# Kernel optimization log

Measured on AMD Instinct MI355X. Metric: run time of the kernel, lower is better.

## Reference

```python
import jax, jax.numpy as jnp
import numpy as np

IMAGE_W = 1024; IMAGE_H = 1024
STRIDES = (8, 16, 32, 64, 128)
TOP_N = 1000; MIN_SCORE = 0.01; NMS_THR = 0.6; MAX_DET = 100
BATCH = 16; NUM_CLASSES = 80


def setup_inputs():
    keys = jax.random.split(jax.random.key(0), 3 * len(STRIDES))
    inp = {}
    for l, s in enumerate(STRIDES):
        H, W = IMAGE_H // s, IMAGE_W // s
        inp[f"cls_head_{l}"] = jax.random.normal(keys[3 * l], (BATCH, H, W, NUM_CLASSES), jnp.float32)
        inp[f"reg_head_{l}"] = jax.random.normal(keys[3 * l + 1], (BATCH, H, W, 4), jnp.float32)
        inp[f"center_head_{l}"] = jax.random.normal(keys[3 * l + 2], (BATCH, H, W, 1), jnp.float32)
        xs = (jnp.arange(W, dtype=jnp.float32) + 0.5) * s
        ys = (jnp.arange(H, dtype=jnp.float32) + 0.5) * s
        gx, gy = jnp.meshgrid(xs, ys)  # each [H, W]
        pos = jnp.stack([gx, gy], axis=-1)  # [H, W, 2] = (ctr_x, ctr_y)
        inp[f"position_{l}"] = jnp.broadcast_to(pos, (BATCH, H, W, 2))
    return inp


def _decode_levels(cls_heads, reg_heads, center_heads, positions):
    S, C, R, P = [], [], [], []
    for cls, reg, ctr, pos in zip(cls_heads, reg_heads, center_heads, positions):
        B = cls.shape[0]
        cls = jax.nn.sigmoid(cls).reshape(B, -1, cls.shape[-1])  # [B,N,C]
        reg = jnp.exp(reg).reshape(B, -1, 4)
        ctr = jax.nn.sigmoid(ctr).reshape(B, -1)
        pos = pos.reshape(B, -1, 2)
        scores = jnp.sqrt(jnp.max(cls, axis=2) * ctr)  # sqrt(cls_max * centerness)
        classes = jnp.argmax(cls, axis=2)
        if scores.shape[1] >= TOP_N:
            scores, idx = jax.lax.top_k(scores, TOP_N)
            classes = jnp.take_along_axis(classes, idx, axis=1)
            reg = jnp.take_along_axis(reg, idx[:, :, None], axis=1)
            pos = jnp.take_along_axis(pos, idx[:, :, None], axis=1)
        S.append(scores); C.append(classes); R.append(reg); P.append(pos)
    return (jnp.concatenate(S, 1), jnp.concatenate(C, 1),
            jnp.concatenate(R, 1), jnp.concatenate(P, 1))


def _nms_keep(boxes, valid, iou_thr):
    # greedy class-agnostic NMS on score-descending boxes [N,4]
    N = boxes.shape[0]
    x1, y1, x2, y2 = boxes[:, 0], boxes[:, 1], boxes[:, 2], boxes[:, 3]
    areas = (x2 - x1) * (y2 - y1)
    idx = jnp.arange(N)

    def body(i, suppressed):
        keep_i = valid[i] & ~suppressed[i]
        xx1 = jnp.maximum(x1[i], x1); yy1 = jnp.maximum(y1[i], y1)
        xx2 = jnp.minimum(x2[i], x2); yy2 = jnp.minimum(y2[i], y2)
        inter = jnp.maximum(xx2 - xx1, 0.0) * jnp.maximum(yy2 - yy1, 0.0)
        iou = inter / (areas[i] + areas - inter)
        return suppressed | (keep_i & (iou > iou_thr) & (idx > i))

    suppressed = jax.lax.fori_loop(0, N, body, jnp.zeros((N,), bool))
    return valid & ~suppressed


def _per_image(scores, classes, reg, pos):
    xy_min = pos - reg[:, 0:2]
    xy_max = pos + reg[:, 2:4]
    boxes = jnp.concatenate([xy_min, xy_max], axis=1).astype(jnp.int32)  # trunc like .int()
    boxes = jnp.stack([jnp.maximum(boxes[:, 0], 0),
                       jnp.maximum(boxes[:, 1], 0),
                       jnp.minimum(boxes[:, 2], IMAGE_W - 1),
                       jnp.minimum(boxes[:, 3], IMAGE_H - 1)], axis=1).astype(jnp.float32)
    valid = scores > MIN_SCORE
    order = jnp.argsort(jnp.where(valid, -scores, jnp.inf))  # valid, score-descending first
    sb, ss = boxes[order], scores[order]
    sc, sv = classes[order].astype(jnp.float32), valid[order]
    kept = _nms_keep(sb, sv, NMS_THR)
    rank = jnp.cumsum(kept) - 1
    slot = jnp.where(kept, jnp.minimum(rank, MAX_DET), MAX_DET)  # overflow -> scratch slot
    out_s = jnp.full((MAX_DET + 1,), -1.0, jnp.float32).at[slot].set(jnp.where(kept, ss, -1.0))[:MAX_DET]
    out_c = jnp.full((MAX_DET + 1,), -1.0, jnp.float32).at[slot].set(jnp.where(kept, sc, -1.0))[:MAX_DET]
    out_b = jnp.full((MAX_DET + 1, 4), -1.0, jnp.float32).at[slot].set(jnp.where(kept[:, None], sb, -1.0))[:MAX_DET]
    return out_s, out_c, out_b


def _forward(cls_heads, reg_heads, center_heads, positions):
    s, c, r, p = _decode_levels(cls_heads, reg_heads, center_heads, positions)
    return jax.vmap(_per_image)(s, c, r, p)


def reference(cls_head_0, reg_head_0, center_head_0, position_0,
              cls_head_1, reg_head_1, center_head_1, position_1,
              cls_head_2, reg_head_2, center_head_2, position_2,
              cls_head_3, reg_head_3, center_head_3, position_3,
              cls_head_4, reg_head_4, center_head_4, position_4):
    cls_heads = [cls_head_0, cls_head_1, cls_head_2, cls_head_3, cls_head_4]
    reg_heads = [reg_head_0, reg_head_1, reg_head_2, reg_head_3, reg_head_4]
    center_heads = [center_head_0, center_head_1, center_head_2, center_head_3, center_head_4]
    positions = [position_0, position_1, position_2, position_3, position_4]
    return _forward(cls_heads, reg_heads, center_heads, positions)
```

## Files before the change

### kernel.cpp

```cpp
#include <hip/hip_runtime.h>
#include <stdint.h>

#define BATCH 16
#define NCLS 80
#define NPOS 21824
#define POOLN 3320
#define MAXDET 100

#define CAP0 4096
#define CAP1 2432
#define CAP2 1024
#define C34 320
#define SEG1 (CAP0)
#define SEG2 (CAP0 + CAP1)
#define SEG3 (CAP0 + CAP1 + CAP2)
#define CAPTOT (SEG3 + C34)

#define DEC_BPI 341
#define POS_BPI 13
#define NBINS 4096

__device__ const int d_lvl_off[5] = {0, 16384, 20480, 21504, 21760};
__device__ const int d_lvl_hw[5]  = {16384, 4096, 1024, 256, 64};

struct Ptrs { const float* p[20]; };

__device__ __forceinline__ void map_lvl(int r, int& level, int& hw) {
  if      (r < 16384) { level = 0; hw = r; }
  else if (r < 20480) { level = 1; hw = r - 16384; }
  else if (r < 21504) { level = 2; hw = r - 20480; }
  else if (r < 21760) { level = 3; hw = r - 21504; }
  else                { level = 4; hw = r - 21760; }
}


__global__ __launch_bounds__(256) void decode_kernel(Ptrs args, uint4* __restrict__ dec,
                                                     unsigned long long* __restrict__ gbuf,
                                                     unsigned* __restrict__ sbuf) {
  __shared__ float2 sm[1280];
  int b  = blockIdx.x / DEC_BPI;
  int bb = blockIdx.x - b * DEC_BPI;
  int t = threadIdx.x;

  int flat0 = bb * 64;
  int level, hw0;
  map_lvl(flat0, level, hw0);
  int HW = d_lvl_hw[level];

  const float* cls = args.p[level * 4 + 0];
  const float* reg = args.p[level * 4 + 1];
  const float* ctr = args.p[level * 4 + 2];
  const float* pos = args.p[level * 4 + 3];

  const float4* c4 = (const float4*)(cls + ((long)b * HW + hw0) * NCLS);
#pragma unroll
  for (int w = 0; w < 5; ++w) {
    int f = t + 256 * w;
    float4 v = c4[f];
    int q = f % 20;
    float m = -1e30f; int am = 4 * q;
    if (v.x > m) { m = v.x; am = 4 * q + 0; }
    if (v.y > m) { m = v.y; am = 4 * q + 1; }
    if (v.z > m) { m = v.z; am = 4 * q + 2; }
    if (v.w > m) { m = v.w; am = 4 * q + 3; }
    sm[f] = make_float2(m, __int_as_float(am));
  }
  __syncthreads();

  int aoff = t >> 2, r = t & 3;
  int base = aoff * 20 + 5 * r;
  float2 c0 = sm[base];
  float m = c0.x; int am = __float_as_int(c0.y);
#pragma unroll
  for (int i = 1; i < 5; ++i) {
    float2 cc = sm[base + i];
    int oa = __float_as_int(cc.y);
    if (cc.x > m || (cc.x == m && oa < am)) { m = cc.x; am = oa; }
  }
#pragma unroll
  for (int d = 1; d <= 2; d <<= 1) {
    float om = __shfl_xor(m, d, 64);
    int   oa = __shfl_xor(am, d, 64);
    if (om > m || (om == m && oa < am)) { m = om; am = oa; }
  }

  if (r == 0) {
    int hw = hw0 + aoff;
    long abase = (long)b * HW + hw;
    float4 rg = *(const float4*)(reg + abase * 4);
    float  ct = ctr[abase];
    float2 ps = ((const float2*)pos)[abase];

    float e0 = expf(rg.x), e1 = expf(rg.y), e2 = expf(rg.z), e3 = expf(rg.w);
    int x1 = (int)(ps.x - e0);
    int y1 = (int)(ps.y - e1);
    int x2 = (int)(ps.x + e2);
    int y2 = (int)(ps.y + e3);
    x1 = max(x1, 0); y1 = max(y1, 0);
    x2 = min(x2, 1023); y2 = min(y2, 1023);

    float sigm = 1.0f / (1.0f + expf(-m));
    float sigc = 1.0f / (1.0f + expf(-ct));
    float score = sqrtf(sigm * sigc);

    uint4 e;
    e.x = __float_as_uint(score);
    e.y = (unsigned)am;
    e.z = (unsigned)(x1 & 0xFFFF) | ((unsigned)y1 << 16);
    e.w = (unsigned)(x2 & 0xFFFF) | ((unsigned)y2 << 16);
    dec[b * NPOS + flat0 + aoff] = e;

    unsigned nsb = ~e.x;
    sbuf[b * NPOS + flat0 + aoff] = nsb;
    if (level >= 3) {
      unsigned long long key =
          ((unsigned long long)nsb << 32) | (unsigned)((level << 20) | hw);
      gbuf[(size_t)b * CAPTOT + SEG3 + ((level == 3) ? hw : 256 + hw)] = key;
    }
  }
}

#define SWQ(q) ((q) ^ (((q) >> 3) & 7))
#define LKI(e) (2 * SWQ((e) >> 1) + ((e) & 1))

__device__ __forceinline__ void cmpswap(unsigned long long& a, unsigned long long& b,
                                        bool asc) {
  unsigned long long mn = a < b ? a : b;
  unsigned long long mx = a < b ? b : a;
  a = asc ? mn : mx;
  b = asc ? mx : mn;
}

__global__ __launch_bounds__(256) void selectsort_kernel(const unsigned* __restrict__ sbuf,
                                                         unsigned long long* __restrict__ gbuf,
                                                         int* __restrict__ gcnt) {
  __shared__ unsigned h[NBINS];
  __shared__ unsigned long long lk[4096];
  __shared__ unsigned wpart[4];
  __shared__ int shB;
  __shared__ int sh_cnt;

  int img = blockIdx.x >> 2, sg = blockIdx.x & 3;
  int t = threadIdx.x, lane = t & 63, wv = t >> 6;
  unsigned long long* gb = gbuf + (size_t)img * CAPTOT;

  int base, cap, n, loff;
  if      (sg == 0) { base = 0;    cap = CAP0; n = 16384; loff = 0; }
  else if (sg == 1) { base = SEG1; cap = CAP1; n = 4096;  loff = 16384; }
  else if (sg == 2) { base = SEG2; cap = CAP2; n = 1024;  loff = 20480; }
  else              { base = SEG3; cap = C34;  n = 0;     loff = 0; }

  int c;
  if (sg < 3) {
    for (int i = t; i < NBINS; i += 256) h[i] = 0;
    if (t == 0) sh_cnt = 0;
    __syncthreads();
    const unsigned* sb = sbuf + img * NPOS + loff;
    for (int i = t; i < n; i += 256) atomicAdd(&h[sb[i] >> 20], 1u);
    __syncthreads();

    unsigned hl[16]; unsigned s = 0;
#pragma unroll
    for (int k = 0; k < 16; ++k) { hl[k] = h[16 * t + k]; s += hl[k]; }
    unsigned incl = s;
    for (int d = 1; d < 64; d <<= 1) {
      unsigned v = __shfl_up(incl, d, 64);
      if (lane >= d) incl += v;
    }
    if (lane == 63) wpart[wv] = incl;
    __syncthreads();
    unsigned woff = 0;
    for (int w = 0; w < wv; ++w) woff += wpart[w];
    unsigned excl = woff + incl - s;
    if (excl < 1000u && excl + s >= 1000u) {
      unsigned cum = excl; int B = NBINS - 1;
#pragma unroll
      for (int k = 0; k < 16; ++k) {
        cum += hl[k];
        if (cum >= 1000u) { B = 16 * t + k; break; }
      }
      shB = B;
    }
    __syncthreads();
    int B = shB;

    for (int i = t; i < n; i += 256) {
      unsigned nsb = sb[i];
      bool sel = (int)(nsb >> 20) <= B;
      unsigned long long msk = __ballot(sel);
      if (msk) {
        int nsel = __popcll(msk);
        int bas = 0;
        if (lane == 0) bas = atomicAdd(&sh_cnt, nsel);
        bas = __shfl(bas, 0, 64);
        if (sel) {
          int p = bas + __popcll(msk & ((1ULL << lane) - 1ULL));
          if (p < cap) {
            unsigned long long key =
                ((unsigned long long)nsb << 32) | (unsigned)((sg << 20) | i);
            lk[LKI(p)] = key;
          }
        }
      }
    }
    __syncthreads();
    c = min(sh_cnt, cap);
    if (t == 0) gcnt[img * 3 + sg] = sh_cnt;
  } else {
    for (int i = t; i < C34; i += 256) lk[LKI(i)] = gb[SEG3 + i];
    c = C34;
    __syncthreads();
  }

  int Pnet = 512;
  while (Pnet < c) Pnet <<= 1;
  for (int e = c + t; e < Pnet; e += 256) lk[LKI(e)] = ~0ULL;
  __syncthreads();

  ulonglong2* lds2 = (ulonglong2*)lk;
  unsigned long long key[16];
  if (t * 16 < Pnet) {
#pragma unroll
    for (int w = 0; w < 8; ++w) {
      ulonglong2 val = lds2[SWQ(t * 8 + w)];
      key[2 * w]     = val.x;
      key[2 * w + 1] = val.y;
    }
  } else {
#pragma unroll
    for (int v = 0; v < 16; ++v) key[v] = ~0ULL;
  }

#pragma unroll
  for (int kk = 2; kk <= 8; kk <<= 1)
#pragma unroll
    for (int j = kk >> 1; j >= 1; j >>= 1)
#pragma unroll
      for (int v = 0; v < 16; ++v)
        if (!(v & j)) cmpswap(key[v], key[v | j], (v & kk) == 0);

  for (int k = 16; k <= Pnet; k <<= 1) {
    bool asc = (t & (k >> 4)) == 0;
    for (int j = k >> 1; j >= 16; j >>= 1) {
      int d = j >> 4;
      bool keep_min = ((t & d) == 0) == asc;
      if (d <= 32) {
#pragma unroll
        for (int v = 0; v < 16; ++v) {
          unsigned long long p = __shfl_xor(key[v], d, 64);
          unsigned long long mn = key[v] < p ? key[v] : p;
          unsigned long long mx = key[v] < p ? p : key[v];
          key[v] = keep_min ? mn : mx;
        }
      } else {
        __syncthreads();
#pragma unroll
        for (int w = 0; w < 8; ++w)
          lds2[SWQ(t * 8 + w)] = make_ulonglong2(key[2 * w], key[2 * w + 1]);
        __syncthreads();
        int tp = t ^ d;
#pragma unroll
        for (int w = 0; w < 8; ++w) {
          ulonglong2 pv = lds2[SWQ(tp * 8 + w)];
          unsigned long long a = key[2 * w], b = key[2 * w + 1];
          unsigned long long mn0 = a < pv.x ? a : pv.x, mx0 = a < pv.x ? pv.x : a;
          unsigned long long mn1 = b < pv.y ? b : pv.y, mx1 = b < pv.y ? pv.y : b;
          key[2 * w]     = keep_min ? mn0 : mx0;
          key[2 * w + 1] = keep_min ? mn1 : mx1;
        }
      }
    }
#pragma unroll
    for (int j = 8; j >= 1; j >>= 1)
#pragma unroll
      for (int v = 0; v < 16; ++v)
        if (!(v & j)) cmpswap(key[v], key[v | j], asc);
  }

  __syncthreads();
  if (t * 16 < Pnet) {
#pragma unroll
    for (int w = 0; w < 8; ++w)
      lds2[SWQ(t * 8 + w)] = make_ulonglong2(key[2 * w], key[2 * w + 1]);
  }
  __syncthreads();
  int npairs = (c + 1) >> 1;
  ulonglong2* gb2 = (ulonglong2*)(gb + base);
  for (int q = t; q < npairs; q += 256) gb2[q] = lds2[SWQ(q)];
}

__device__ __forceinline__ int lbound(const unsigned long long* __restrict__ a,
                                      int n, unsigned long long x) {
  int lo = 0, len = n;
  while (len > 0) {
    int half = len >> 1;
    int mid = lo + half;
    if (a[mid] < x) { lo = mid + 1; len -= half + 1; }
    else            { len = half; }
  }
  return lo;
}

__global__ __launch_bounds__(256) void pos_kernel(const unsigned long long* __restrict__ gbuf,
                                                  const int* __restrict__ gcnt,
                                                  unsigned long long* __restrict__ pool) {
  int img = blockIdx.x / POS_BPI, bb = blockIdx.x % POS_BPI;
  int e = bb * 256 + threadIdx.x;
  const unsigned long long* gb = gbuf + (size_t)img * CAPTOT;

  int c0 = min(gcnt[img * 3 + 0], CAP0);
  int c1 = min(gcnt[img * 3 + 1], CAP1);
  int c2 = min(gcnt[img * 3 + 2], CAP2);
  int m0 = min(c0, 1000), m1 = min(c1, 1000), m2 = min(c2, 1000);
  int tot = m0 + m1 + m2 + C34;
  if (e >= tot) return;

  int t, i;
  if      (e < m0)           { t = 0; i = e; }
  else if (e < m0 + m1)      { t = 1; i = e - m0; }
  else if (e < m0 + m1 + m2) { t = 2; i = e - m0 - m1; }
  else                       { t = 3; i = e - m0 - m1 - m2; }

  const int off[4] = {0, SEG1, SEG2, SEG3};
  const int cc[4]  = {c0, c1, c2, C34};

  unsigned long long key = gb[off[t] + i];
  int pos = i;
#pragma unroll
  for (int u = 0; u < 4; ++u) {
    if (u == t) continue;
    pos += min(lbound(gb + off[u], cc[u], key), 1000);
  }
  pool[img * POOLN + pos] = key;
}

__global__ __launch_bounds__(64) void nms_kernel(const uint4* __restrict__ dec,
                                                 const unsigned long long* __restrict__ pool,
                                                 float* __restrict__ out) {
  __shared__ int4 kbox[MAXDET];
  __shared__ int  karea[MAXDET];
  int img = blockIdx.x;
  int lane = threadIdx.x;

  float* out_s = out + img * MAXDET;
  float* out_c = out + BATCH * MAXDET + img * MAXDET;
  float* out_b = out + 2 * BATCH * MAXDET + img * MAXDET * 4;

  int k = 0;
  bool full = false;

  for (int b0 = 0; b0 < POOLN; b0 += 64) {
    int i = b0 + lane;
    bool inb = i < POOLN;

    float sc = -1.0f;
    int4 bx = make_int4(0, 0, 0, 0);
    int ar = 0;
    unsigned cls = 0;
    if (inb) {
      unsigned long long key = pool[img * POOLN + i];
      unsigned low = (unsigned)key;
      int level = (low >> 20) & 7;
      int idx = low & 0xFFFFF;
      uint4 e = dec[img * NPOS + d_lvl_off[level] + idx];
      sc = __uint_as_float(e.x);
      cls = e.y;
      bx = make_int4((int)(e.z & 0xFFFF), (int)(e.z >> 16),
                     (int)(e.w & 0xFFFF), (int)(e.w >> 16));
      ar = (bx.z - bx.x) * (bx.w - bx.y);
    }

    bool invalid = !(sc > 0.01f);
    if (__all(invalid)) break;
    bool sup = invalid;

    for (int t = 0; t < k; ++t) {
      int4 kb = kbox[t];
      int  ka = karea[t];
      int xx1 = max(bx.x, kb.x), yy1 = max(bx.y, kb.y);
      int xx2 = min(bx.z, kb.z), yy2 = min(bx.w, kb.w);
      int iw = max(xx2 - xx1, 0), ih = max(yy2 - yy1, 0);
      int inter = iw * ih;
      int uni = ar + ka - inter;
      sup = sup || (((long long)inter << 25) > 20132661LL * (long long)uni);
    }

    unsigned long long alive = __ballot(!sup);
    while (alive) {
      int j = __ffsll(alive) - 1;

      int jx1 = __shfl(bx.x, j, 64), jy1 = __shfl(bx.y, j, 64);
      int jx2 = __shfl(bx.z, j, 64), jy2 = __shfl(bx.w, j, 64);
      int ja  = __shfl(ar,   j, 64);

      if (lane == j) {
        kbox[k]  = bx;
        karea[k] = ar;
        out_s[k] = sc;
        out_c[k] = (float)(int)cls;
        out_b[k * 4 + 0] = (float)bx.x;
        out_b[k * 4 + 1] = (float)bx.y;
        out_b[k * 4 + 2] = (float)bx.z;
        out_b[k * 4 + 3] = (float)bx.w;
      }
      ++k;
      if (k == MAXDET) { full = true; break; }

      if (lane > j) {
        int xx1 = max(bx.x, jx1), yy1 = max(bx.y, jy1);
        int xx2 = min(bx.z, jx2), yy2 = min(bx.w, jy2);
        int iw = max(xx2 - xx1, 0), ih = max(yy2 - yy1, 0);
        int inter = iw * ih;
        int uni = ar + ja - inter;
        sup = sup || (((long long)inter << 25) > 20132661LL * (long long)uni);
      }

      unsigned long long himask = (j < 63) ? (~0ULL << (j + 1)) : 0ULL;
      alive = __ballot(!sup) & himask;
    }
    if (full) break;
  }

  for (int s = k + lane; s < MAXDET; s += 64) {
    out_s[s] = -1.0f;
    out_c[s] = -1.0f;
    out_b[s * 4 + 0] = -1.0f;
    out_b[s * 4 + 1] = -1.0f;
    out_b[s * 4 + 2] = -1.0f;
    out_b[s * 4 + 3] = -1.0f;
  }
}

extern "C" void kernel_launch(void* const* d_in, const int* in_sizes, int n_in,
                              void* d_out, int out_size, void* d_ws, size_t ws_size,
                              hipStream_t stream) {
  Ptrs args;
  for (int i = 0; i < 20; ++i) args.p[i] = (const float*)d_in[i];

  char* ws = (char*)d_ws;
  uint4* dec = (uint4*)ws;
  ws += (size_t)BATCH * NPOS * 16;
  unsigned long long* pool = (unsigned long long*)ws;
  ws += (size_t)BATCH * POOLN * 8;
  unsigned long long* gbuf = (unsigned long long*)ws;
  ws += (size_t)BATCH * CAPTOT * 8;
  unsigned* sbuf = (unsigned*)ws;
  ws += (size_t)BATCH * NPOS * 4;
  int* gcnt = (int*)ws;
  float* out = (float*)d_out;

  decode_kernel<<<BATCH * DEC_BPI, 256, 0, stream>>>(args, dec, gbuf, sbuf);
  selectsort_kernel<<<BATCH * 4, 256, 0, stream>>>(sbuf, gbuf, gcnt);
  pos_kernel<<<BATCH * POS_BPI, 256, 0, stream>>>(gbuf, gcnt, pool);
  nms_kernel<<<BATCH, 64, 0, stream>>>(dec, pool, out);
}
```

Baseline: 308.4 us.

## Widen selectsort to 1024 threads and full-sort smaller levels without histogram

The select-and-sort kernel now runs 1024 threads per block, each holding 4 keys in registers instead of 16. This spreads the bitonic sort and the histogram work over more lanes in a launch of only 64 blocks. Levels 1 and 2 skip the histogram threshold step and bitonic-sort all their candidates, writing only up to the segment capacity. That trades a larger sort on level 1 for fewer passes and barriers. Level 0 loads its 16 elements per thread up front with unrolled loops.

```diff
diff --git a/kernel.cpp b/kernel.cpp
--- a/kernel.cpp
+++ b/kernel.cpp
@@ -131,12 +131,12 @@
   b = asc ? mx : mn;
 }
 
-__global__ __launch_bounds__(256) void selectsort_kernel(const unsigned* __restrict__ sbuf,
-                                                         unsigned long long* __restrict__ gbuf,
-                                                         int* __restrict__ gcnt) {
+__global__ __launch_bounds__(1024) void selectsort_kernel(const unsigned* __restrict__ sbuf,
+                                                          unsigned long long* __restrict__ gbuf,
+                                                          int* __restrict__ gcnt) {
   __shared__ unsigned h[NBINS];
   __shared__ unsigned long long lk[4096];
-  __shared__ unsigned wpart[4];
+  __shared__ unsigned wpart[16];
   __shared__ int shB;
   __shared__ int sh_cnt;
 
@@ -144,24 +144,24 @@
   int t = threadIdx.x, lane = t & 63, wv = t >> 6;
   unsigned long long* gb = gbuf + (size_t)img * CAPTOT;
 
-  int base, cap, n, loff;
-  if      (sg == 0) { base = 0;    cap = CAP0; n = 16384; loff = 0; }
-  else if (sg == 1) { base = SEG1; cap = CAP1; n = 4096;  loff = 16384; }
-  else if (sg == 2) { base = SEG2; cap = CAP2; n = 1024;  loff = 20480; }
-  else              { base = SEG3; cap = C34;  n = 0;     loff = 0; }
-
-  int c;
-  if (sg < 3) {
-    for (int i = t; i < NBINS; i += 256) h[i] = 0;
+  int c, base, cap;
+  if (sg == 0) {
+    base = 0; cap = CAP0;
+    const unsigned* sb = sbuf + img * NPOS;
+
+    for (int i = t; i < NBINS; i += 1024) h[i] = 0;
     if (t == 0) sh_cnt = 0;
     __syncthreads();
-    const unsigned* sb = sbuf + img * NPOS + loff;
-    for (int i = t; i < n; i += 256) atomicAdd(&h[sb[i] >> 20], 1u);
+    unsigned dig[16];
+#pragma unroll
+    for (int w = 0; w < 16; ++w) dig[w] = sb[t + 1024 * w] >> 20;
+#pragma unroll
+    for (int w = 0; w < 16; ++w) atomicAdd(&h[dig[w]], 1u);
     __syncthreads();
 
-    unsigned hl[16]; unsigned s = 0;
-#pragma unroll
-    for (int k = 0; k < 16; ++k) { hl[k] = h[16 * t + k]; s += hl[k]; }
+    unsigned hl[4]; unsigned s = 0;
+#pragma unroll
+    for (int k2 = 0; k2 < 4; ++k2) { hl[k2] = h[4 * t + k2]; s += hl[k2]; }
     unsigned incl = s;
     for (int d = 1; d < 64; d <<= 1) {
       unsigned v = __shfl_up(incl, d, 64);
@@ -175,17 +175,22 @@
     if (excl < 1000u && excl + s >= 1000u) {
       unsigned cum = excl; int B = NBINS - 1;
 #pragma unroll
-      for (int k = 0; k < 16; ++k) {
-        cum += hl[k];
-        if (cum >= 1000u) { B = 16 * t + k; break; }
+      for (int k2 = 0; k2 < 4; ++k2) {
+        cum += hl[k2];
+        if (cum >= 1000u) { B = 4 * t + k2; break; }
       }
       shB = B;
     }
     __syncthreads();
     int B = shB;
 
-    for (int i = t; i < n; i += 256) {
-      unsigned nsb = sb[i];
+    unsigned nsbv[16];
+#pragma unroll
+    for (int w = 0; w < 16; ++w) nsbv[w] = sb[t + 1024 * w];
+#pragma unroll
+    for (int w = 0; w < 16; ++w) {
+      int i = t + 1024 * w;
+      unsigned nsb = nsbv[w];
       bool sel = (int)(nsb >> 20) <= B;
       unsigned long long msk = __ballot(sel);
       if (msk) {
@@ -196,8 +201,7 @@
         if (sel) {
           int p = bas + __popcll(msk & ((1ULL << lane) - 1ULL));
           if (p < cap) {
-            unsigned long long key =
-                ((unsigned long long)nsb << 32) | (unsigned)((sg << 20) | i);
+            unsigned long long key = ((unsigned long long)nsb << 32) | (unsigned)i;
             lk[LKI(p)] = key;
           }
         }
@@ -205,48 +209,47 @@
     }
     __syncthreads();
     c = min(sh_cnt, cap);
-    if (t == 0) gcnt[img * 3 + sg] = sh_cnt;
+    if (t == 0) gcnt[img * 3] = sh_cnt;
+  } else if (sg < 3) {
+    int n, loff;
+    if (sg == 1) { base = SEG1; cap = CAP1; n = 4096; loff = 16384; }
+    else         { base = SEG2; cap = CAP2; n = 1024; loff = 20480; }
+    const unsigned* sb = sbuf + img * NPOS + loff;
+    for (int i = t; i < n; i += 1024)
+      lk[LKI(i)] = ((unsigned long long)sb[i] << 32) | (unsigned)((sg << 20) | i);
+    c = n;
+    if (t == 0) gcnt[img * 3 + sg] = n;
   } else {
-    for (int i = t; i < C34; i += 256) lk[LKI(i)] = gb[SEG3 + i];
+    base = SEG3; cap = C34;
+    for (int i = t; i < C34; i += 1024) lk[LKI(i)] = gb[SEG3 + i];
     c = C34;
-    __syncthreads();
   }
 
   int Pnet = 512;
   while (Pnet < c) Pnet <<= 1;
-  for (int e = c + t; e < Pnet; e += 256) lk[LKI(e)] = ~0ULL;
+  for (int e = c + t; e < Pnet; e += 1024) lk[LKI(e)] = ~0ULL;
   __syncthreads();
 
   ulonglong2* lds2 = (ulonglong2*)lk;
-  unsigned long long key[16];
-  if (t * 16 < Pnet) {
-#pragma unroll
-    for (int w = 0; w < 8; ++w) {
-      ulonglong2 val = lds2[SWQ(t * 8 + w)];
-      key[2 * w]     = val.x;
-      key[2 * w + 1] = val.y;
-    }
+  unsigned long long key[4];
+  if (t * 4 < Pnet) {
+    ulonglong2 v0 = lds2[SWQ(2 * t)], v1 = lds2[SWQ(2 * t + 1)];
+    key[0] = v0.x; key[1] = v0.y; key[2] = v1.x; key[3] = v1.y;
   } else {
-#pragma unroll
-    for (int v = 0; v < 16; ++v) key[v] = ~0ULL;
-  }
-
-#pragma unroll
-  for (int kk = 2; kk <= 8; kk <<= 1)
-#pragma unroll
-    for (int j = kk >> 1; j >= 1; j >>= 1)
-#pragma unroll
-      for (int v = 0; v < 16; ++v)
-        if (!(v & j)) cmpswap(key[v], key[v | j], (v & kk) == 0);
-
-  for (int k = 16; k <= Pnet; k <<= 1) {
-    bool asc = (t & (k >> 4)) == 0;
-    for (int j = k >> 1; j >= 16; j >>= 1) {
-      int d = j >> 4;
+    key[0] = key[1] = key[2] = key[3] = ~0ULL;
+  }
+
+  cmpswap(key[0], key[1], true);
+  cmpswap(key[2], key[3], false);
+
+  for (int k = 4; k <= Pnet; k <<= 1) {
+    bool asc = (t & (k >> 2)) == 0;
+    for (int j = k >> 1; j >= 4; j >>= 1) {
+      int d = j >> 2;
       bool keep_min = ((t & d) == 0) == asc;
       if (d <= 32) {
 #pragma unroll
-        for (int v = 0; v < 16; ++v) {
+        for (int v = 0; v < 4; ++v) {
           unsigned long long p = __shfl_xor(key[v], d, 64);
           unsigned long long mn = key[v] < p ? key[v] : p;
           unsigned long long mx = key[v] < p ? p : key[v];
@@ -254,39 +257,35 @@
         }
       } else {
         __syncthreads();
-#pragma unroll
-        for (int w = 0; w < 8; ++w)
-          lds2[SWQ(t * 8 + w)] = make_ulonglong2(key[2 * w], key[2 * w + 1]);
+        lds2[SWQ(2 * t)]     = make_ulonglong2(key[0], key[1]);
+        lds2[SWQ(2 * t + 1)] = make_ulonglong2(key[2], key[3]);
         __syncthreads();
         int tp = t ^ d;
-#pragma unroll
-        for (int w = 0; w < 8; ++w) {
-          ulonglong2 pv = lds2[SWQ(tp * 8 + w)];
-          unsigned long long a = key[2 * w], b = key[2 * w + 1];
-          unsigned long long mn0 = a < pv.x ? a : pv.x, mx0 = a < pv.x ? pv.x : a;
-          unsigned long long mn1 = b < pv.y ? b : pv.y, mx1 = b < pv.y ? pv.y : b;
-          key[2 * w]     = keep_min ? mn0 : mx0;
-          key[2 * w + 1] = keep_min ? mn1 : mx1;
-        }
+        ulonglong2 p0 = lds2[SWQ(2 * tp)], p1 = lds2[SWQ(2 * tp + 1)];
+        unsigned long long pv0 = p0.x, pv1 = p0.y, pv2 = p1.x, pv3 = p1.y;
+        unsigned long long mn, mx;
+        mn = key[0] < pv0 ? key[0] : pv0; mx = key[0] < pv0 ? pv0 : key[0];
+        key[0] = keep_min ? mn : mx;
+        mn = key[1] < pv1 ? key[1] : pv1; mx = key[1] < pv1 ? pv1 : key[1];
+        key[1] = keep_min ? mn : mx;
+        mn = key[2] < pv2 ? key[2] : pv2; mx = key[2] < pv2 ? pv2 : key[2];
+        key[2] = keep_min ? mn : mx;
+        mn = key[3] < pv3 ? key[3] : pv3; mx = key[3] < pv3 ? pv3 : key[3];
+        key[3] = keep_min ? mn : mx;
       }
     }
-#pragma unroll
-    for (int j = 8; j >= 1; j >>= 1)
-#pragma unroll
-      for (int v = 0; v < 16; ++v)
-        if (!(v & j)) cmpswap(key[v], key[v | j], asc);
+    cmpswap(key[0], key[2], asc); cmpswap(key[1], key[3], asc);
+    cmpswap(key[0], key[1], asc); cmpswap(key[2], key[3], asc);
   }
 
   __syncthreads();
-  if (t * 16 < Pnet) {
-#pragma unroll
-    for (int w = 0; w < 8; ++w)
-      lds2[SWQ(t * 8 + w)] = make_ulonglong2(key[2 * w], key[2 * w + 1]);
-  }
+  lds2[SWQ(2 * t)]     = make_ulonglong2(key[0], key[1]);
+  lds2[SWQ(2 * t + 1)] = make_ulonglong2(key[2], key[3]);
   __syncthreads();
-  int npairs = (c + 1) >> 1;
+  int c_out = min(c, cap);
+  int npairs = (c_out + 1) >> 1;
   ulonglong2* gb2 = (ulonglong2*)(gb + base);
-  for (int q = t; q < npairs; q += 256) gb2[q] = lds2[SWQ(q)];
+  for (int q = t; q < npairs; q += 1024) gb2[q] = lds2[SWQ(q)];
 }
 
 __device__ __forceinline__ int lbound(const unsigned long long* __restrict__ a,
@@ -450,7 +449,7 @@
   float* out = (float*)d_out;
 
   decode_kernel<<<BATCH * DEC_BPI, 256, 0, stream>>>(args, dec, gbuf, sbuf);
-  selectsort_kernel<<<BATCH * 4, 256, 0, stream>>>(sbuf, gbuf, gcnt);
+  selectsort_kernel<<<BATCH * 4, 1024, 0, stream>>>(sbuf, gbuf, gcnt);
   pos_kernel<<<BATCH * POS_BPI, 256, 0, stream>>>(gbuf, gcnt, pool);
   nms_kernel<<<BATCH, 64, 0, stream>>>(dec, pool, out);
 }
```

New measurement: 266.8 us. -13.5%, faster.
